# Kernel tuning notes

Hardware: AMD Instinct MI355X
Metric: run time of the kernel (lower is better)

Reference implementation:

```python
import jax, jax.numpy as jnp
import numpy as np

USER_NUM = 100000
ITEM_NUM = 50000
N = USER_NUM + ITEM_NUM
D = 64
NNZ = 2400000
B = 4096
NLEVEL = 3
LEAF = 32
HID = 256
NCLS = 2
NLAYERS = 2
EPS = 0.1
TAU = 0.2


def _l2norm(x, axis=-1):
    return x / jnp.clip(jnp.linalg.norm(x, axis=axis, keepdims=True), 1e-12)


def setup_inputs():
    key = jax.random.key(0)
    ks = jax.random.split(key, 32)
    def w(k, shape):
        fan = shape[-2] if len(shape) >= 2 else shape[-1]
        return jax.random.normal(k, shape, jnp.float32) / np.sqrt(fan)
    z = lambda *s: jnp.zeros(s, jnp.float32)
    return {
        "ego_emb": w(ks[0], (N, D)),
        "gc_w": w(ks[1], (NLAYERS, D, D)), "gc_b": z(NLAYERS, D),
        "bi_w": w(ks[2], (NLAYERS, D, D)), "bi_b": z(NLAYERS, D),
        "uh_w": w(ks[3], (NLEVEL, D, D)), "uh_b": z(NLEVEL, D),
        "ih_w": w(ks[4], (NLEVEL, D, D)), "ih_b": z(NLEVEL, D),
        "ud_w1": w(ks[5], (NLEVEL, D, HID)), "ud_b1": z(NLEVEL, HID),
        "ud_w2": w(ks[6], (NLEVEL, HID, LEAF)), "ud_b2": z(NLEVEL, LEAF),
        "id_w1": w(ks[7], (NLEVEL, D, HID)), "id_b1": z(NLEVEL, HID),
        "id_w2": w(ks[8], (NLEVEL, HID, LEAF)), "id_b2": z(NLEVEL, LEAF),
        "q_w": w(ks[9], (LEAF, LEAF)), "q_b": z(LEAF),
        "k_w": w(ks[10], (LEAF, LEAF)), "k_b": z(LEAF),
        "v_w": w(ks[11], (LEAF, LEAF)), "v_b": z(LEAF),
        "dg_w1": w(ks[12], (NLEVEL * LEAF, D)), "dg_b1": z(D),
        "dg_w2": w(ks[13], (D, D)), "dg_b2": z(D),
        "pr_w": w(ks[14], (D, NCLS)), "pr_b": z(NCLS),
        "adj_vals": jax.random.uniform(ks[15], (NNZ,), jnp.float32) / 16.0,
        "hier_skills": jax.random.uniform(ks[16], (B, NLEVEL * LEAF), jnp.float32),
        "user_id": jax.random.randint(ks[17], (B,), 0, USER_NUM),
        "item_id": jax.random.randint(ks[18], (B,), 0, ITEM_NUM),
        "adj_rows": jax.random.randint(ks[19], (NNZ,), 0, N),
        "adj_cols": jax.random.randint(ks[20], (NNZ,), 0, N),
    }


def _sam(x, q_w, q_b, k_w, k_b, v_w, v_b):
    # x: [B, S, d], single-head self-attention (n_heads=1)
    d = x.shape[-1]
    q = x @ q_w + q_b
    k = x @ k_w + k_b
    v = x @ v_w + v_b
    scores = jnp.einsum('bsd,btd->bst', q, k) / jnp.sqrt(jnp.float32(d))
    attn = jax.nn.softmax(scores, axis=-1)  # softmax over key axis t
    return jnp.einsum('bst,btd->bsd', attn, v)


def _cl_loss(v1, v2):
    n1 = _l2norm(v1)
    n2 = _l2norm(v2)
    pos = jnp.exp(jnp.sum(n1 * n2, -1) / TAU)
    ttl = jnp.sum(jnp.exp(n1 @ n2.T / TAU), axis=1)
    return jnp.mean(-jnp.log(pos / ttl))


def _cl_module(recs, key):
    # recs: [L, B, LEAF]
    noise = jax.random.uniform(key, recs.shape, recs.dtype)
    recs_new = recs + jnp.sign(recs) * _l2norm(noise) * EPS
    return jnp.mean(jax.vmap(_cl_loss)(recs, recs_new))


def reference(ego_emb, gc_w, gc_b, bi_w, bi_b, uh_w, uh_b, ih_w, ih_b,
              ud_w1, ud_b1, ud_w2, ud_b2, id_w1, id_b1, id_w2, id_b2,
              q_w, q_b, k_w, k_b, v_w, v_b, dg_w1, dg_b1, dg_w2, dg_b2,
              pr_w, pr_b, adj_vals, hier_skills, user_id, item_id,
              adj_rows, adj_cols):
    # ---- NGCF propagation: sparse adj matmul + bi-interaction ----
    E = ego_emb
    E_sum = ego_emb
    for l in range(NLAYERS):
        side = jax.ops.segment_sum(adj_vals[:, None] * E[adj_cols], adj_rows,
                                   num_segments=N)  # spmm(adj_norm, E)
        sum_e = jax.nn.leaky_relu(side @ gc_w[l] + gc_b[l])
        bi_e = jax.nn.leaky_relu((E * side) @ bi_w[l] + bi_b[l])
        E = _l2norm(sum_e + bi_e)  # dropout -> identity (eval)
        E_sum = E_sum + E
    ue = E_sum[:USER_NUM][user_id]   # [B, D]
    ie = E_sum[USER_NUM:][item_id]   # [B, D]
    # ---- hierarchy projections + disentangled encoders (stacked over levels) ----
    u_reps = jnp.tanh(jnp.einsum('bd,lde->lbe', ue, uh_w) + uh_b[:, None, :])
    i_reps = jnp.tanh(jnp.einsum('bd,lde->lbe', ie, ih_w) + ih_b[:, None, :])
    u_recs = jnp.einsum('lbh,lhk->lbk',
                        jnp.tanh(jnp.einsum('lbd,ldh->lbh', u_reps, ud_w1) + ud_b1[:, None, :]),
                        ud_w2) + ud_b2[:, None, :]  # [L, B, LEAF]
    i_recs = jnp.einsum('lbh,lhk->lbk',
                        jnp.tanh(jnp.einsum('lbd,ldh->lbh', i_reps, id_w1) + id_b1[:, None, :]),
                        id_w2) + id_b2[:, None, :]
    # ---- self-attention across levels ----
    u_att = _sam(u_recs.transpose(1, 0, 2), q_w, q_b, k_w, k_b, v_w, v_b)  # [B, L, LEAF]
    i_att = _sam(i_recs.transpose(1, 0, 2), q_w, q_b, k_w, k_b, v_w, v_b)
    # ---- contrastive losses (detached in original via torch.Tensor(...)) ----
    kc = jax.random.split(jax.random.key(42), 2)
    cl = _cl_module(u_att.transpose(1, 0, 2), kc[0]) + _cl_module(i_att.transpose(1, 0, 2), kc[1])
    cl = jax.lax.stop_gradient(cl)
    # ---- diagnosis head ----
    skills = hier_skills.reshape(B, NLEVEL, LEAF)
    diag = ((jax.nn.sigmoid(u_att) - jax.nn.sigmoid(i_att)) * skills).reshape(B, NLEVEL * LEAF)
    h = jnp.tanh(diag @ dg_w1 + dg_b1) @ dg_w2 + dg_b2  # dropout -> identity (eval)
    out = jax.nn.softmax(h @ pr_w + pr_b, axis=-1)
    return (out, cl)
```

## Files before the change

kernel.cpp:

```cpp
#include <hip/hip_runtime.h>
#include <stdint.h>
#include <math.h>

#define USER_N 100000
#define NODE_N 150000
#define DD 64
#define NNZE 2400000
#define BB 4096
#define NLV 3
#define LF 32
#define HALF_SZ 196608u
#define NTILE 586
#define NSUB 8
#define SCAP 1024
#define EPB 4096
#define LCAP 5120

typedef __attribute__((ext_vector_type(8))) short bf16x8;
typedef __attribute__((ext_vector_type(4))) float f32x4;
typedef __attribute__((ext_vector_type(2))) float f32x2;

#define XCC_ID_IMM 63508

__host__ __device__ inline void tf_block(uint32_t k0, uint32_t k1, uint32_t& x0, uint32_t& x1) {
  uint32_t ks[3] = {k0, k1, k0 ^ k1 ^ 0x1BD11BDAu};
  x0 += ks[0]; x1 += ks[1];
  const int R0[4] = {13, 15, 26, 6};
  const int R1[4] = {17, 29, 16, 24};
#pragma unroll
  for (int i = 0; i < 5; ++i) {
    const int* R = (i & 1) ? R1 : R0;
#pragma unroll
    for (int j = 0; j < 4; ++j) {
      x0 += x1;
      x1 = (x1 << R[j]) | (x1 >> (32 - R[j]));
      x1 ^= x0;
    }
    x0 += ks[(i + 1) % 3];
    x1 += ks[(i + 2) % 3] + (uint32_t)(i + 1);
  }
}

__device__ inline float tf_uniform(uint32_t ka, uint32_t kb, uint32_t m) {
  uint32_t x0, x1;
  bool first = m < HALF_SZ;
  if (first) { x0 = m; x1 = m + HALF_SZ; } else { x0 = m - HALF_SZ; x1 = m; }
  tf_block(ka, kb, x0, x1);
  uint32_t bits = first ? x0 : x1;
  return __uint_as_float((bits >> 9) | 0x3f800000u) - 1.0f;
}

__device__ inline unsigned short f2bf(float x) {
  uint32_t b = __float_as_uint(x);
  return (unsigned short)((b + 0x7FFFu + ((b >> 16) & 1u)) >> 16);
}

__device__ inline unsigned char f2fp8(float x) {
  return (unsigned char)(__builtin_amdgcn_cvt_pk_fp8_f32(x, x, 0, false) & 0xFF);
}

__device__ inline void fp8_fma(float4& acc, uint2 rec, uint32_t wrd) {
  float vv = __uint_as_float(rec.y);
  f32x2 lo = __builtin_amdgcn_cvt_pk_f32_fp8((int)wrd, false);
  f32x2 hi = __builtin_amdgcn_cvt_pk_f32_fp8((int)wrd, true);
  acc.x = fmaf(vv, lo.x, acc.x);
  acc.y = fmaf(vv, lo.y, acc.y);
  acc.z = fmaf(vv, hi.x, acc.z);
  acc.w = fmaf(vv, hi.y, acc.w);
}

__global__ __launch_bounds__(256) void k_init(
    const float* __restrict__ ego, uint32_t* __restrict__ E8,
    const float* __restrict__ uh_w, const float* __restrict__ ud_w1,
    const float* __restrict__ ud_w2, const float* __restrict__ ih_w,
    const float* __restrict__ id_w1, const float* __restrict__ id_w2,
    unsigned short* __restrict__ s1t, unsigned short* __restrict__ s2t,
    unsigned short* __restrict__ s3t, int* __restrict__ cursor,
    float* __restrict__ clbuf) {
  if (blockIdx.x >= 10047) {
    int i = (blockIdx.x - 10047) * 256 + threadIdx.x;
    if (i < NTILE * NSUB * 16) cursor[i] = 0;
    if (i == 0) { clbuf[0] = 0.f; ((int*)clbuf)[1] = 0; }
    return;
  }
  if (blockIdx.x < 9375) {
    int i = blockIdx.x * 256 + threadIdx.x;
    float4 v = ((const float4*)ego)[i];
    int w01 = __builtin_amdgcn_cvt_pk_fp8_f32(v.x, v.y, 0, false);
    int w = __builtin_amdgcn_cvt_pk_fp8_f32(v.z, v.w, w01, true);
    E8[i] = (uint32_t)w;
    return;
  }
  int i = (blockIdx.x - 9375) * 256 + threadIdx.x;
  if (i < 24576) {
    int sl = i >> 12, r = i & 4095, e = r >> 6, d = r & 63;
    const float* src = (sl >= 3 ? ih_w : uh_w);
    int l = sl % 3;
    s1t[i] = f2bf(src[l * 4096 + d * 64 + e]);
  } else if (i < 24576 + 98304) {
    int j = i - 24576;
    int sl = j >> 14, r = j & 16383, e = r >> 6, d = r & 63;
    const float* src = (sl >= 3 ? id_w1 : ud_w1);
    int l = sl % 3;
    s2t[j] = f2bf(src[l * 16384 + d * 256 + e]);
  } else if (i < 172032) {
    int j = i - 24576 - 98304;
    int sl = j >> 13, r = j & 8191, e = r >> 8, d = r & 255;
    const float* src = (sl >= 3 ? id_w2 : ud_w2);
    int l = sl % 3;
    s3t[j] = f2bf(src[l * 8192 + d * 32 + e]);
  }
}

__global__ __launch_bounds__(256) void k_scatter_t(const int* __restrict__ rows,
                                                   const int* __restrict__ cols,
                                                   const float* __restrict__ vals,
                                                   int* __restrict__ cursor,
                                                   uint2* __restrict__ sedge_r) {
  __shared__ int cnt[NTILE];
  __shared__ int binbase[NTILE];
  __shared__ int gbase[NTILE];
  __shared__ int partial[256];
  __shared__ uint2 staged[EPB];
  __shared__ unsigned short tileof[EPB];
  int t = threadIdx.x;
  for (int i = t; i < NTILE; i += 256) cnt[i] = 0;
  __syncthreads();
  int ebase = blockIdx.x * EPB;
  int r[16], rk[16];
#pragma unroll
  for (int j = 0; j < 16; ++j) {
    int e = ebase + j * 256 + t;
    r[j] = (e < NNZE) ? rows[e] : -1;
    rk[j] = (r[j] >= 0) ? atomicAdd(&cnt[r[j] >> 8], 1) : 0;
  }
  __syncthreads();
  int b0 = t * 3;
  int own = (b0 < NTILE) ? ((NTILE - b0 < 3) ? (NTILE - b0) : 3) : 0;
  int s0 = 0;
  for (int k = 0; k < own; ++k) s0 += cnt[b0 + k];
  partial[t] = s0;
  __syncthreads();
  for (int off = 1; off < 256; off <<= 1) {
    int add = (t >= off) ? partial[t - off] : 0;
    __syncthreads();
    partial[t] += add;
    __syncthreads();
  }
  int excl = partial[t] - s0;
  unsigned myx = __builtin_amdgcn_s_getreg(XCC_ID_IMM) & (NSUB - 1);
  {
    int run = excl;
    for (int k = 0; k < own; ++k) {
      int b = b0 + k;
      int c = cnt[b];
      binbase[b] = run;
      gbase[b] = c ? atomicAdd(&cursor[(b * NSUB + (int)myx) * 16], c) : 0;
      run += c;
    }
  }
  __syncthreads();
#pragma unroll
  for (int j = 0; j < 16; ++j) {
    if (r[j] < 0) continue;
    int e = ebase + j * 256 + t;
    int tile = r[j] >> 8;
    int pos = binbase[tile] + rk[j];
    staged[pos] = make_uint2((uint32_t)cols[e] | ((uint32_t)(r[j] & 255) << 18),
                             __float_as_uint(vals[e]));
    tileof[pos] = (unsigned short)tile;
  }
  __syncthreads();
  int nrec = NNZE - ebase;
  if (nrec > EPB) nrec = EPB;
  for (int i = t; i < nrec; i += 256) {
    int tile = tileof[i];
    int q = i - binbase[tile];
    int p = gbase[tile] + q;
    uint2 rec = staged[i];
    if (p < SCAP) {
      sedge_r[(size_t)(tile * NSUB + (int)myx) * SCAP + p] = rec;
    } else {
#pragma unroll 1
      for (int att = 1; att < NSUB; ++att) {
        int seg = tile * NSUB + (int)((myx + att) & (NSUB - 1));
        int p2 = atomicAdd(&cursor[seg * 16], 1);
        if (p2 < SCAP) { sedge_r[(size_t)seg * SCAP + p2] = rec; break; }
      }
    }
  }
}

__global__ __launch_bounds__(256) void k_sort_t(const uint2* __restrict__ sedge_r,
                                                const int* __restrict__ cursor,
                                                uint2* __restrict__ sedge,
                                                int* __restrict__ row_start) {
  __shared__ int hist[256], buf[256], curs[256];
  __shared__ int obase_s;
  __shared__ uint2 staged[LCAP];
  int t = threadIdx.x;
  int tile = blockIdx.x;
  if (t == 0) obase_s = 0;
  hist[t] = 0;
  __syncthreads();
  int ob = 0;
  for (int i = t; i < tile * NSUB; i += 256) {
    int c = cursor[i * 16];
    ob += (c < SCAP) ? c : SCAP;
  }
  if (ob) atomicAdd(&obase_s, ob);
  int segcnt[NSUB];
#pragma unroll
  for (int x = 0; x < NSUB; ++x) {
    int c = cursor[(tile * NSUB + x) * 16];
    segcnt[x] = (c < SCAP) ? c : SCAP;
  }
#pragma unroll 1
  for (int x = 0; x < NSUB; ++x) {
    const uint2* sp = sedge_r + (size_t)(tile * NSUB + x) * SCAP;
    for (int i = t; i < segcnt[x]; i += 256)
      atomicAdd(&hist[sp[i].x >> 18], 1);
  }
  __syncthreads();
  int obase = obase_s;
  int v = hist[t];
  buf[t] = v;
  __syncthreads();
  for (int off = 1; off < 256; off <<= 1) {
    int add = (t >= off) ? buf[t - off] : 0;
    __syncthreads();
    buf[t] += add;
    __syncthreads();
  }
  int total = buf[255];
  int excl = buf[t] - v;
  curs[t] = excl;
  int row = tile * 256 + t;
  if (row < NODE_N) row_start[row] = obase + excl;
  if (tile == NTILE - 1 && t == 0) row_start[NODE_N] = NNZE;
  __syncthreads();
#pragma unroll 1
  for (int x = 0; x < NSUB; ++x) {
    const uint2* sp = sedge_r + (size_t)(tile * NSUB + x) * SCAP;
    for (int i = t; i < segcnt[x]; i += 256) {
      uint2 rec = sp[i];
      int rl = rec.x >> 18;
      int p = atomicAdd(&curs[rl], 1);
      uint2 outrec = make_uint2(rec.x & 0x3FFFFu, rec.y);
      if (p < LCAP) staged[p] = outrec;
      else sedge[obase + p] = outrec;
    }
  }
  __syncthreads();
  int n = (total < LCAP) ? total : LCAP;
  for (int i = t; i < n; i += 256)
    sedge[obase + i] = staged[i];
}

__global__ __launch_bounds__(256) void k_spmm(const uint32_t* __restrict__ E8,
                                              const uint2* __restrict__ sedge,
                                              const int* __restrict__ row_start,
                                              unsigned short* __restrict__ side16,
                                              unsigned short* __restrict__ p16) {
  int r = blockIdx.x * 4 + (threadIdx.x >> 6);
  int lane = threadIdx.x & 63;
  int g = lane >> 4;
  int q = lane & 15;
  int rs = row_start[r], re = row_start[r + 1];
  float4 acc = make_float4(0.f, 0.f, 0.f, 0.f);
  int e = rs;
  for (; e + 16 <= re; e += 16) {
    uint2 e0 = sedge[e + g];
    uint2 e1 = sedge[e + 4 + g];
    uint2 e2 = sedge[e + 8 + g];
    uint2 e3 = sedge[e + 12 + g];
    uint32_t a0 = E8[(size_t)e0.x * 16 + q];
    uint32_t a1 = E8[(size_t)e1.x * 16 + q];
    uint32_t a2 = E8[(size_t)e2.x * 16 + q];
    uint32_t a3 = E8[(size_t)e3.x * 16 + q];
    fp8_fma(acc, e0, a0);
    fp8_fma(acc, e1, a1);
    fp8_fma(acc, e2, a2);
    fp8_fma(acc, e3, a3);
  }
  for (; e + 8 <= re; e += 8) {
    uint2 e0 = sedge[e + g];
    uint2 e1 = sedge[e + 4 + g];
    uint32_t a0 = E8[(size_t)e0.x * 16 + q];
    uint32_t a1 = E8[(size_t)e1.x * 16 + q];
    fp8_fma(acc, e0, a0);
    fp8_fma(acc, e1, a1);
  }
  for (; e + 4 <= re; e += 4) {
    uint2 e0 = sedge[e + g];
    uint32_t a0 = E8[(size_t)e0.x * 16 + q];
    fp8_fma(acc, e0, a0);
  }
  for (; e < re; ++e) {
    if (g == (e & 3)) {
      uint2 e0 = sedge[e];
      uint32_t a0 = E8[(size_t)e0.x * 16 + q];
      fp8_fma(acc, e0, a0);
    }
  }
#pragma unroll
  for (int off = 16; off <= 32; off <<= 1) {
    acc.x += __shfl_xor(acc.x, off, 64);
    acc.y += __shfl_xor(acc.y, off, 64);
    acc.z += __shfl_xor(acc.z, off, 64);
    acc.w += __shfl_xor(acc.w, off, 64);
  }
  if (g == 0) {
    uint32_t ew = E8[(size_t)r * 16 + q];
    f32x2 elo = __builtin_amdgcn_cvt_pk_f32_fp8((int)ew, false);
    f32x2 ehi = __builtin_amdgcn_cvt_pk_f32_fp8((int)ew, true);
    ushort4 s16, pp;
    s16.x = f2bf(acc.x); s16.y = f2bf(acc.y); s16.z = f2bf(acc.z); s16.w = f2bf(acc.w);
    pp.x = f2bf(acc.x * elo.x); pp.y = f2bf(acc.y * elo.y);
    pp.z = f2bf(acc.z * ehi.x); pp.w = f2bf(acc.w * ehi.y);
    *(ushort4*)&side16[(size_t)r * DD + q * 4] = s16;
    *(ushort4*)&p16[(size_t)r * DD + q * 4] = pp;
  }
}

__global__ __launch_bounds__(256) void k_transform(const float* __restrict__ gw,
                                                   const float* __restrict__ gb,
                                                   const float* __restrict__ bw,
                                                   const float* __restrict__ bb,
                                                   const unsigned short* __restrict__ side16,
                                                   const unsigned short* __restrict__ p16,
                                                   float* __restrict__ Eout,
                                                   unsigned char* __restrict__ E8b) {
  int t = threadIdx.x;
  int wv = t >> 6, lane = t & 63;
  int n = lane & 15, quad = lane >> 4;
  bf16x8 wg[4][2], wb[4][2];
  float gbl[4], bbl[4];
#pragma unroll
  for (int c = 0; c < 4; ++c) {
    gbl[c] = gb[c * 16 + n];
    bbl[c] = bb[c * 16 + n];
#pragma unroll
    for (int h = 0; h < 2; ++h) {
#pragma unroll
      for (int j = 0; j < 8; ++j) {
        int k = h * 32 + quad * 8 + j;
        wg[c][h][j] = (short)f2bf(gw[k * 64 + c * 16 + n]);
        wb[c][h][j] = (short)f2bf(bw[k * 64 + c * 16 + n]);
      }
    }
  }
  const f32x4 z = {0.f, 0.f, 0.f, 0.f};
  for (int tile = blockIdx.x * 4 + wv; tile < NODE_N / 16; tile += gridDim.x * 4) {
    int i0 = tile * 16;
    bf16x8 as0 = *(const bf16x8*)&side16[(size_t)(i0 + n) * DD + quad * 8];
    bf16x8 as1 = *(const bf16x8*)&side16[(size_t)(i0 + n) * DD + 32 + quad * 8];
    bf16x8 ap0 = *(const bf16x8*)&p16[(size_t)(i0 + n) * DD + quad * 8];
    bf16x8 ap1 = *(const bf16x8*)&p16[(size_t)(i0 + n) * DD + 32 + quad * 8];
    float v[4][4];
    float sq0 = 0.f, sq1 = 0.f, sq2 = 0.f, sq3 = 0.f;
#pragma unroll
    for (int c = 0; c < 4; ++c) {
      f32x4 ag = __builtin_amdgcn_mfma_f32_16x16x32_bf16(as0, wg[c][0], z, 0, 0, 0);
      ag = __builtin_amdgcn_mfma_f32_16x16x32_bf16(as1, wg[c][1], ag, 0, 0, 0);
      f32x4 ab = __builtin_amdgcn_mfma_f32_16x16x32_bf16(ap0, wb[c][0], z, 0, 0, 0);
      ab = __builtin_amdgcn_mfma_f32_16x16x32_bf16(ap1, wb[c][1], ab, 0, 0, 0);
#pragma unroll
      for (int r = 0; r < 4; ++r) {
        float a1 = ag[r] + gbl[c];
        a1 = (a1 > 0.f) ? a1 : 0.01f * a1;
        float a2 = ab[r] + bbl[c];
        a2 = (a2 > 0.f) ? a2 : 0.01f * a2;
        float vv = a1 + a2;
        v[c][r] = vv;
        if (r == 0) sq0 += vv * vv;
        else if (r == 1) sq1 += vv * vv;
        else if (r == 2) sq2 += vv * vv;
        else sq3 += vv * vv;
      }
    }
#pragma unroll
    for (int off = 1; off < 16; off <<= 1) {
      sq0 += __shfl_xor(sq0, off, 64);
      sq1 += __shfl_xor(sq1, off, 64);
      sq2 += __shfl_xor(sq2, off, 64);
      sq3 += __shfl_xor(sq3, off, 64);
    }
    float inv0 = 1.f / fmaxf(sqrtf(sq0), 1e-12f);
    float inv1 = 1.f / fmaxf(sqrtf(sq1), 1e-12f);
    float inv2 = 1.f / fmaxf(sqrtf(sq2), 1e-12f);
    float inv3 = 1.f / fmaxf(sqrtf(sq3), 1e-12f);
#pragma unroll
    for (int c = 0; c < 4; ++c) {
      float vn0 = v[c][0] * inv0;
      float vn1 = v[c][1] * inv1;
      float vn2 = v[c][2] * inv2;
      float vn3 = v[c][3] * inv3;
      size_t o0 = (size_t)(i0 + quad * 4 + 0) * DD + c * 16 + n;
      size_t o1 = o0 + DD, o2 = o1 + DD, o3 = o2 + DD;
      Eout[o0] = vn0; Eout[o1] = vn1; Eout[o2] = vn2; Eout[o3] = vn3;
      E8b[o0] = f2fp8(vn0); E8b[o1] = f2fp8(vn1);
      E8b[o2] = f2fp8(vn2); E8b[o3] = f2fp8(vn3);
    }
  }
}

__global__ __launch_bounds__(256) void k_encoder6(
    const float* __restrict__ ego, const float* __restrict__ E1,
    const float* __restrict__ E2, const int* __restrict__ uid,
    const int* __restrict__ iid,
    const unsigned short* __restrict__ s1t, const unsigned short* __restrict__ s2t,
    const unsigned short* __restrict__ s3t,
    const float* __restrict__ uh_b, const float* __restrict__ ud_b1,
    const float* __restrict__ ud_b2, const float* __restrict__ ih_b,
    const float* __restrict__ id_b1, const float* __restrict__ id_b2,
    float* __restrict__ recs_u, float* __restrict__ recs_i) {
  __shared__ unsigned short X[32][72];
  __shared__ unsigned short R1[32][64];
  __shared__ unsigned short T[32][256];
  int t = threadIdx.x;
  int w = t >> 6, lane = t & 63;
  int n = lane & 15, quad = lane >> 4;
  int trow = w & 1;
  int cg = w >> 1;
  int r0 = blockIdx.x * 32;
  int l = blockIdx.y, side = blockIdx.z;
  int sl = side * 3 + l;
  const float* hb = side ? ih_b : uh_b;
  const float* bb1 = side ? id_b1 : ud_b1;
  const float* bb2 = side ? id_b2 : ud_b2;
  float* recs = side ? recs_i : recs_u;
  const f32x4 z = {0.f, 0.f, 0.f, 0.f};

  {
    int row = t >> 3;
    int c0 = (t & 7) * 8;
    int node = side ? (USER_N + iid[r0 + row]) : uid[r0 + row];
    const float* pe = ego + (size_t)node * 64 + c0;
    const float* p1 = E1 + (size_t)node * 64 + c0;
    const float* p2 = E2 + (size_t)node * 64 + c0;
#pragma unroll
    for (int j = 0; j < 8; ++j)
      X[row][c0 + j] = f2bf(pe[j] + p1[j] + p2[j]);
  }
  __syncthreads();

  {
    bf16x8 a0 = *(const bf16x8*)&X[trow * 16 + n][quad * 8];
    bf16x8 a1 = *(const bf16x8*)&X[trow * 16 + n][32 + quad * 8];
    const unsigned short* Wt = s1t + (size_t)sl * 4096;
#pragma unroll
    for (int cc = 0; cc < 2; ++cc) {
      int cb = cg * 2 + cc;
      bf16x8 wb0 = *(const bf16x8*)&Wt[(size_t)(cb * 16 + n) * 64 + quad * 8];
      bf16x8 wb1 = *(const bf16x8*)&Wt[(size_t)(cb * 16 + n) * 64 + 32 + quad * 8];
      f32x4 acc = __builtin_amdgcn_mfma_f32_16x16x32_bf16(a0, wb0, z, 0, 0, 0);
      acc = __builtin_amdgcn_mfma_f32_16x16x32_bf16(a1, wb1, acc, 0, 0, 0);
      float bias = hb[l * 64 + cb * 16 + n];
#pragma unroll
      for (int r = 0; r < 4; ++r)
        R1[trow * 16 + quad * 4 + r][cb * 16 + n] = f2bf(tanhf(acc[r] + bias));
    }
  }
  __syncthreads();

  {
    bf16x8 a0 = *(const bf16x8*)&R1[trow * 16 + n][quad * 8];
    bf16x8 a1 = *(const bf16x8*)&R1[trow * 16 + n][32 + quad * 8];
    const unsigned short* Wt = s2t + (size_t)sl * 16384;
#pragma unroll
    for (int cc = 0; cc < 8; ++cc) {
      int cb = cg * 8 + cc;
      bf16x8 wb0 = *(const bf16x8*)&Wt[(size_t)(cb * 16 + n) * 64 + quad * 8];
      bf16x8 wb1 = *(const bf16x8*)&Wt[(size_t)(cb * 16 + n) * 64 + 32 + quad * 8];
      f32x4 acc = __builtin_amdgcn_mfma_f32_16x16x32_bf16(a0, wb0, z, 0, 0, 0);
      acc = __builtin_amdgcn_mfma_f32_16x16x32_bf16(a1, wb1, acc, 0, 0, 0);
      float bias = bb1[l * 256 + cb * 16 + n];
#pragma unroll
      for (int r = 0; r < 4; ++r)
        T[trow * 16 + quad * 4 + r][cb * 16 + n] = f2bf(tanhf(acc[r] + bias));
    }
  }
  __syncthreads();

  {
    const unsigned short* Wt = s3t + (size_t)sl * 8192;
    f32x4 acc = z;
#pragma unroll
    for (int h = 0; h < 8; ++h) {
      bf16x8 a = *(const bf16x8*)&T[trow * 16 + n][h * 32 + quad * 8];
      bf16x8 b = *(const bf16x8*)&Wt[(size_t)(cg * 16 + n) * 256 + h * 32 + quad * 8];
      acc = __builtin_amdgcn_mfma_f32_16x16x32_bf16(a, b, acc, 0, 0, 0);
    }
    float bias = bb2[l * 32 + cg * 16 + n];
#pragma unroll
    for (int r = 0; r < 4; ++r)
      recs[((size_t)l * BB + (r0 + trow * 16 + quad * 4 + r)) * 32 + cg * 16 + n] =
          acc[r] + bias;
  }
}

__global__ __launch_bounds__(256) void k_attnz(const float* __restrict__ recs_u,
                                               const float* __restrict__ recs_i,
                                               const float* __restrict__ qw, const float* __restrict__ qb,
                                               const float* __restrict__ kw, const float* __restrict__ kb,
                                               const float* __restrict__ vw, const float* __restrict__ vb,
                                               uint32_t ku0, uint32_t ku1, uint32_t ki0, uint32_t ki1,
                                               float* __restrict__ att_u, float* __restrict__ att_i,
                                               unsigned short* __restrict__ n1b,
                                               unsigned short* __restrict__ n2b,
                                               float* __restrict__ posdot) {
  int side = blockIdx.y;
  const float* recs = side ? recs_i : recs_u;
  float* att = side ? att_i : att_u;
  uint32_t ka = side ? ki0 : ku0;
  uint32_t kb2 = side ? ki1 : ku1;
  int t = threadIdx.x;
  int b = blockIdx.x * 8 + (t >> 5);
  int d = t & 31;
  float x0 = recs[((size_t)0 * BB + b) * 32 + d];
  float x1 = recs[((size_t)1 * BB + b) * 32 + d];
  float x2 = recs[((size_t)2 * BB + b) * 32 + d];
  float q0 = qb[d], q1 = q0, q2 = q0;
  float c0 = kb[d], c1 = c0, c2 = c0;
  float v0 = vb[d], v1 = v0, v2 = v0;
#pragma unroll 4
  for (int kk = 0; kk < 32; ++kk) {
    float xa = __shfl(x0, kk, 32);
    float xb = __shfl(x1, kk, 32);
    float xc = __shfl(x2, kk, 32);
    float wq = qw[kk * 32 + d], wk = kw[kk * 32 + d], wv = vw[kk * 32 + d];
    q0 += xa * wq; q1 += xb * wq; q2 += xc * wq;
    c0 += xa * wk; c1 += xb * wk; c2 += xc * wk;
    v0 += xa * wv; v1 += xb * wv; v2 += xc * wv;
  }
  float qs[3] = {q0, q1, q2}, ks[3] = {c0, c1, c2}, vs[3] = {v0, v1, v2};
  float sc[3][3];
#pragma unroll
  for (int s = 0; s < 3; ++s)
#pragma unroll
    for (int u = 0; u < 3; ++u) {
      float p = qs[s] * ks[u];
#pragma unroll
      for (int off = 16; off; off >>= 1) p += __shfl_xor(p, off, 32);
      sc[s][u] = p * 0.17677669529663687f;
    }
#pragma unroll
  for (int s = 0; s < 3; ++s) {
    float m = fmaxf(sc[s][0], fmaxf(sc[s][1], sc[s][2]));
    float e0 = __expf(sc[s][0] - m), e1 = __expf(sc[s][1] - m), e2 = __expf(sc[s][2] - m);
    float inv = 1.f / (e0 + e1 + e2);
    float r = (e0 * vs[0] + e1 * vs[1] + e2 * vs[2]) * inv;
    att[(size_t)b * 96 + s * 32 + d] = r;
    float ss = r * r;
#pragma unroll
    for (int off = 16; off; off >>= 1) ss += __shfl_xor(ss, off, 32);
    float nv1 = r / fmaxf(sqrtf(ss), 1e-12f);
    uint32_t mm = ((uint32_t)(s * BB + b)) * 32u + (uint32_t)d;
    float u = tf_uniform(ka, kb2, mm);
    float us = u * u;
#pragma unroll
    for (int off = 16; off; off >>= 1) us += __shfl_xor(us, off, 32);
    float un = u / fmaxf(sqrtf(us), 1e-12f);
    float sgn = (r > 0.f) ? 1.f : ((r < 0.f) ? -1.f : 0.f);
    float rn = r + sgn * un * 0.1f;
    float s2 = rn * rn;
#pragma unroll
    for (int off = 16; off; off >>= 1) s2 += __shfl_xor(s2, off, 32);
    float nv2 = rn / fmaxf(sqrtf(s2), 1e-12f);
    float pd = nv1 * nv2;
#pragma unroll
    for (int off = 16; off; off >>= 1) pd += __shfl_xor(pd, off, 32);
    int g = side * (NLV * BB) + s * BB + b;
    size_t o = (size_t)g * 32 + d;
    n1b[o] = f2bf(nv1);
    n2b[o] = f2bf(nv2);
    if (d == 0) posdot[g] = pd;
  }
}

__global__ __launch_bounds__(256) void k_ttl(const unsigned short* __restrict__ n1b,
                                             const unsigned short* __restrict__ n2b,
                                             const float* __restrict__ posdot,
                                             float* __restrict__ clbuf,
                                             float* __restrict__ outp) {
  __shared__ float ws[4];
  int t = threadIdx.x;
  int wv = t >> 6, lane = t & 63;
  int sl = blockIdx.x >> 6;
  int istripe = blockIdx.x & 63;
  int i0 = istripe * 64 + wv * 16;
  const unsigned short* ab = n1b + (size_t)sl * BB * 32;
  const unsigned short* bb = n2b + (size_t)sl * BB * 32;
  int m = lane & 15, quad = lane >> 4;
  bf16x8 afrag = *(const bf16x8*)&ab[(size_t)(i0 + m) * 32 + quad * 8];
  float r0a = 0.f, r1a = 0.f, r2a = 0.f, r3a = 0.f;
  f32x4 z = {0.f, 0.f, 0.f, 0.f};
  for (int jt = 0; jt < 256; jt += 4) {
    bf16x8 b0 = *(const bf16x8*)&bb[((size_t)((jt + 0) * 16 + m)) * 32 + quad * 8];
    bf16x8 b1 = *(const bf16x8*)&bb[((size_t)((jt + 1) * 16 + m)) * 32 + quad * 8];
    bf16x8 b2 = *(const bf16x8*)&bb[((size_t)((jt + 2) * 16 + m)) * 32 + quad * 8];
    bf16x8 b3 = *(const bf16x8*)&bb[((size_t)((jt + 3) * 16 + m)) * 32 + quad * 8];
    f32x4 s0 = __builtin_amdgcn_mfma_f32_16x16x32_bf16(afrag, b0, z, 0, 0, 0);
    f32x4 s1 = __builtin_amdgcn_mfma_f32_16x16x32_bf16(afrag, b1, z, 0, 0, 0);
    f32x4 s2 = __builtin_amdgcn_mfma_f32_16x16x32_bf16(afrag, b2, z, 0, 0, 0);
    f32x4 s3 = __builtin_amdgcn_mfma_f32_16x16x32_bf16(afrag, b3, z, 0, 0, 0);
    r0a += __expf(s0.x * 5.f) + __expf(s1.x * 5.f) + __expf(s2.x * 5.f) + __expf(s3.x * 5.f);
    r1a += __expf(s0.y * 5.f) + __expf(s1.y * 5.f) + __expf(s2.y * 5.f) + __expf(s3.y * 5.f);
    r2a += __expf(s0.z * 5.f) + __expf(s1.z * 5.f) + __expf(s2.z * 5.f) + __expf(s3.z * 5.f);
    r3a += __expf(s0.w * 5.f) + __expf(s1.w * 5.f) + __expf(s2.w * 5.f) + __expf(s3.w * 5.f);
  }
#pragma unroll
  for (int off = 1; off < 16; off <<= 1) {
    r0a += __shfl_xor(r0a, off, 64);
    r1a += __shfl_xor(r1a, off, 64);
    r2a += __shfl_xor(r2a, off, 64);
    r3a += __shfl_xor(r3a, off, 64);
  }
  float part = 0.f;
  if (m == 0) {
    int rbase = sl * BB + i0 + quad * 4;
    part = (logf(r0a) - posdot[rbase + 0] * 5.0f)
         + (logf(r1a) - posdot[rbase + 1] * 5.0f)
         + (logf(r2a) - posdot[rbase + 2] * 5.0f)
         + (logf(r3a) - posdot[rbase + 3] * 5.0f);
  }
#pragma unroll
  for (int off = 1; off < 64; off <<= 1)
    part += __shfl_xor(part, off, 64);
  if (lane == 0) ws[wv] = part;
  __syncthreads();
  if (t == 0) {
    float blk = ws[0] + ws[1] + ws[2] + ws[3];
    atomicAdd(&clbuf[0], blk);
    __threadfence();
    int done = atomicAdd((int*)&clbuf[1], 1);
    if (done == 383) {
      float total = atomicAdd(&clbuf[0], 0.0f);
      outp[2 * BB] = total * (1.f / 12288.f);
    }
  }
}

__global__ __launch_bounds__(256) void k_head(const float* __restrict__ att_u,
                                              const float* __restrict__ att_i,
                                              const float* __restrict__ skills,
                                              const float* __restrict__ w1, const float* __restrict__ b1,
                                              const float* __restrict__ w2, const float* __restrict__ b2,
                                              const float* __restrict__ pw, const float* __restrict__ pb,
                                              float* __restrict__ outp) {
  __shared__ float diag[4][96], t1[4][64];
  int t = threadIdx.x;
  int w = t >> 6, lane = t & 63;
  int b = blockIdx.x * 4 + w;
  for (int j = lane; j < 96; j += 64) {
    float su = 1.f / (1.f + __expf(-att_u[(size_t)b * 96 + j]));
    float si = 1.f / (1.f + __expf(-att_i[(size_t)b * 96 + j]));
    diag[w][j] = (su - si) * skills[(size_t)b * 96 + j];
  }
  __syncthreads();
  float a = b1[lane];
#pragma unroll 8
  for (int j = 0; j < 96; ++j) a += diag[w][j] * w1[j * 64 + lane];
  t1[w][lane] = tanhf(a);
  __syncthreads();
  float h = b2[lane];
#pragma unroll 8
  for (int kk = 0; kk < 64; ++kk) h += t1[w][kk] * w2[kk * 64 + lane];
  float p0 = h * pw[lane * 2 + 0];
  float p1 = h * pw[lane * 2 + 1];
#pragma unroll
  for (int off = 32; off; off >>= 1) {
    p0 += __shfl_xor(p0, off, 64);
    p1 += __shfl_xor(p1, off, 64);
  }
  if (lane == 0) {
    float l0 = p0 + pb[0], l1 = p1 + pb[1];
    float m = fmaxf(l0, l1);
    float e0 = __expf(l0 - m), e1 = __expf(l1 - m);
    float inv = 1.f / (e0 + e1);
    outp[(size_t)b * 2 + 0] = e0 * inv;
    outp[(size_t)b * 2 + 1] = e1 * inv;
  }
}

extern "C" void kernel_launch(void* const* d_in, const int* in_sizes, int n_in,
                              void* d_out, int out_size, void* d_ws, size_t ws_size,
                              hipStream_t stream) {
  const float* ego    = (const float*)d_in[0];
  const float* gc_w   = (const float*)d_in[1];
  const float* gc_b   = (const float*)d_in[2];
  const float* bi_w   = (const float*)d_in[3];
  const float* bi_b   = (const float*)d_in[4];
  const float* uh_w   = (const float*)d_in[5];
  const float* uh_b   = (const float*)d_in[6];
  const float* ih_w   = (const float*)d_in[7];
  const float* ih_b   = (const float*)d_in[8];
  const float* ud_w1  = (const float*)d_in[9];
  const float* ud_b1  = (const float*)d_in[10];
  const float* ud_w2  = (const float*)d_in[11];
  const float* ud_b2  = (const float*)d_in[12];
  const float* id_w1  = (const float*)d_in[13];
  const float* id_b1  = (const float*)d_in[14];
  const float* id_w2  = (const float*)d_in[15];
  const float* id_b2  = (const float*)d_in[16];
  const float* q_w    = (const float*)d_in[17];
  const float* q_b    = (const float*)d_in[18];
  const float* k_w    = (const float*)d_in[19];
  const float* k_b    = (const float*)d_in[20];
  const float* v_w    = (const float*)d_in[21];
  const float* v_b    = (const float*)d_in[22];
  const float* dg_w1  = (const float*)d_in[23];
  const float* dg_b1  = (const float*)d_in[24];
  const float* dg_w2  = (const float*)d_in[25];
  const float* dg_b2  = (const float*)d_in[26];
  const float* pr_w   = (const float*)d_in[27];
  const float* pr_b   = (const float*)d_in[28];
  const float* adj_vals = (const float*)d_in[29];
  const float* skills = (const float*)d_in[30];
  const int* user_id  = (const int*)d_in[31];
  const int* item_id  = (const int*)d_in[32];
  const int* adj_rows = (const int*)d_in[33];
  const int* adj_cols = (const int*)d_in[34];
  float* outp = (float*)d_out;

  char* w = (char*)d_ws;
  auto alloc = [&](size_t bytes) -> char* {
    char* p = w;
    w += (bytes + 255) & ~(size_t)255;
    return p;
  };
  float* E1     = (float*)alloc((size_t)NODE_N * DD * 4);
  float* E2     = (float*)alloc((size_t)NODE_N * DD * 4);
  uint32_t* E8  = (uint32_t*)alloc((size_t)NODE_N * DD);
  unsigned short* side16 = (unsigned short*)alloc((size_t)NODE_N * DD * 2);
  unsigned short* p16    = (unsigned short*)alloc((size_t)NODE_N * DD * 2);
  uint2* sedge_r= (uint2*)alloc((size_t)NTILE * NSUB * SCAP * 8);
  uint2* sedge  = (uint2*)alloc((size_t)NNZE * 8);
  int*   cursor = (int*)  alloc((size_t)NTILE * NSUB * 16 * 4);
  int*   row_start = (int*)alloc((size_t)(NODE_N + 1) * 4);
  float* posdot = (float*)alloc((size_t)6 * BB * 4);
  float* clbuf  = (float*)alloc(256);
  unsigned short* s1t = (unsigned short*)alloc((size_t)24576 * 2);
  unsigned short* s2t = (unsigned short*)alloc((size_t)98304 * 2);
  unsigned short* s3t = (unsigned short*)alloc((size_t)49152 * 2);

  char* ap = (char*)sedge_r;
  auto alias = [&](size_t bytes) -> char* {
    char* p = ap;
    ap += (bytes + 255) & ~(size_t)255;
    return p;
  };
  float* recs_u = (float*)alias((size_t)NLV * BB * 32 * 4);
  float* recs_i = (float*)alias((size_t)NLV * BB * 32 * 4);
  float* att_u  = (float*)alias((size_t)BB * 96 * 4);
  float* att_i  = (float*)alias((size_t)BB * 96 * 4);
  unsigned short* n1b = (unsigned short*)alias((size_t)6 * BB * 32 * 2);
  unsigned short* n2b = (unsigned short*)alias((size_t)6 * BB * 32 * 2);

  uint32_t a0 = 0, a1 = 2, b0 = 1, b1 = 3;
  tf_block(0u, 42u, a0, a1);
  tf_block(0u, 42u, b0, b1);
  uint32_t ku0 = a0, ku1 = b0;
  uint32_t ki0 = a1, ki1 = b1;

  k_init<<<10341, 256, 0, stream>>>(ego, E8, uh_w, ud_w1, ud_w2,
                                    ih_w, id_w1, id_w2, s1t, s2t, s3t,
                                    cursor, clbuf);
  k_scatter_t<<<(NNZE + EPB - 1) / EPB, 256, 0, stream>>>(adj_rows, adj_cols, adj_vals,
                                                          cursor, sedge_r);
  k_sort_t<<<NTILE, 256, 0, stream>>>(sedge_r, cursor, sedge, row_start);

  float* Ebufs[2] = {E1, E2};
  for (int l = 0; l < 2; ++l) {
    k_spmm<<<37500, 256, 0, stream>>>(E8, sedge, row_start, side16, p16);
    k_transform<<<1172, 256, 0, stream>>>(gc_w + l * 4096, gc_b + l * 64,
                                          bi_w + l * 4096, bi_b + l * 64,
                                          side16, p16, Ebufs[l], (unsigned char*)E8);
  }

  dim3 ge(128, 3, 2);
  k_encoder6<<<ge, 256, 0, stream>>>(ego, E1, E2, user_id, item_id,
                                     s1t, s2t, s3t,
                                     uh_b, ud_b1, ud_b2, ih_b, id_b1, id_b2,
                                     recs_u, recs_i);

  dim3 ga(512, 2);
  k_attnz<<<ga, 256, 0, stream>>>(recs_u, recs_i, q_w, q_b, k_w, k_b, v_w, v_b,
                                  ku0, ku1, ki0, ki1,
                                  att_u, att_i, n1b, n2b, posdot);

  k_ttl<<<384, 256, 0, stream>>>(n1b, n2b, posdot, clbuf, outp);

  k_head<<<1024, 256, 0, stream>>>(att_u, att_i, skills, dg_w1, dg_b1, dg_w2, dg_b2,
                                   pr_w, pr_b, outp);
}
```

Before: 515.1 us.

## Fuse SpMM aggregation with dense layer transform via shared-memory staging

Merges the sparse aggregation kernel and the MFMA transform kernel into one kernel per layer. Each block aggregates 16 rows into LDS as bf16 and then runs the 64x64 transform and L2 normalization directly on them. This removes the side16/p16 round trip through global memory. Weights are pre-transposed to bf16 once in the init kernel, and the fp8 embedding buffer is double-buffered so the fused kernel never reads rows it is also writing. In exchange, each wave handles four rows serially and the block must synchronize before the MFMA phase, which can reduce latency hiding in the gather.

```diff
diff --git a/kernel.cpp b/kernel.cpp
--- a/kernel.cpp
+++ b/kernel.cpp
@@ -74,11 +74,12 @@
     const float* __restrict__ uh_w, const float* __restrict__ ud_w1,
     const float* __restrict__ ud_w2, const float* __restrict__ ih_w,
     const float* __restrict__ id_w1, const float* __restrict__ id_w2,
+    const float* __restrict__ gc_w, const float* __restrict__ bi_w,
     unsigned short* __restrict__ s1t, unsigned short* __restrict__ s2t,
-    unsigned short* __restrict__ s3t, int* __restrict__ cursor,
-    float* __restrict__ clbuf) {
-  if (blockIdx.x >= 10047) {
-    int i = (blockIdx.x - 10047) * 256 + threadIdx.x;
+    unsigned short* __restrict__ s3t, unsigned short* __restrict__ twt,
+    int* __restrict__ cursor, float* __restrict__ clbuf) {
+  if (blockIdx.x >= 10111) {
+    int i = (blockIdx.x - 10111) * 256 + threadIdx.x;
     if (i < NTILE * NSUB * 16) cursor[i] = 0;
     if (i == 0) { clbuf[0] = 0.f; ((int*)clbuf)[1] = 0; }
     return;
@@ -109,6 +110,17 @@
     const float* src = (sl >= 3 ? id_w2 : ud_w2);
     int l = sl % 3;
     s3t[j] = f2bf(src[l * 8192 + d * 32 + e]);
+  } else if (i < 172032 + 16384) {
+    int j = i - 172032;
+    int m = j >> 13;
+    int rest = j & 8191;
+    int l = rest >> 12;
+    int e = rest & 4095;
+    int jj = e & 7, quad = (e >> 3) & 3, h = (e >> 5) & 1;
+    int n = (e >> 6) & 15, c = e >> 10;
+    int k = h * 32 + quad * 8 + jj;
+    const float* src = m ? bi_w : gc_w;
+    twt[j] = f2bf(src[l * 4096 + k * 64 + c * 16 + n]);
   }
 }
 
@@ -257,151 +269,137 @@
     sedge[obase + i] = staged[i];
 }
 
-__global__ __launch_bounds__(256) void k_spmm(const uint32_t* __restrict__ E8,
-                                              const uint2* __restrict__ sedge,
-                                              const int* __restrict__ row_start,
-                                              unsigned short* __restrict__ side16,
-                                              unsigned short* __restrict__ p16) {
-  int r = blockIdx.x * 4 + (threadIdx.x >> 6);
-  int lane = threadIdx.x & 63;
-  int g = lane >> 4;
-  int q = lane & 15;
-  int rs = row_start[r], re = row_start[r + 1];
-  float4 acc = make_float4(0.f, 0.f, 0.f, 0.f);
-  int e = rs;
-  for (; e + 16 <= re; e += 16) {
-    uint2 e0 = sedge[e + g];
-    uint2 e1 = sedge[e + 4 + g];
-    uint2 e2 = sedge[e + 8 + g];
-    uint2 e3 = sedge[e + 12 + g];
-    uint32_t a0 = E8[(size_t)e0.x * 16 + q];
-    uint32_t a1 = E8[(size_t)e1.x * 16 + q];
-    uint32_t a2 = E8[(size_t)e2.x * 16 + q];
-    uint32_t a3 = E8[(size_t)e3.x * 16 + q];
-    fp8_fma(acc, e0, a0);
-    fp8_fma(acc, e1, a1);
-    fp8_fma(acc, e2, a2);
-    fp8_fma(acc, e3, a3);
-  }
-  for (; e + 8 <= re; e += 8) {
-    uint2 e0 = sedge[e + g];
-    uint2 e1 = sedge[e + 4 + g];
-    uint32_t a0 = E8[(size_t)e0.x * 16 + q];
-    uint32_t a1 = E8[(size_t)e1.x * 16 + q];
-    fp8_fma(acc, e0, a0);
-    fp8_fma(acc, e1, a1);
-  }
-  for (; e + 4 <= re; e += 4) {
-    uint2 e0 = sedge[e + g];
-    uint32_t a0 = E8[(size_t)e0.x * 16 + q];
-    fp8_fma(acc, e0, a0);
-  }
-  for (; e < re; ++e) {
-    if (g == (e & 3)) {
-      uint2 e0 = sedge[e];
-      uint32_t a0 = E8[(size_t)e0.x * 16 + q];
-      fp8_fma(acc, e0, a0);
-    }
-  }
-#pragma unroll
-  for (int off = 16; off <= 32; off <<= 1) {
-    acc.x += __shfl_xor(acc.x, off, 64);
-    acc.y += __shfl_xor(acc.y, off, 64);
-    acc.z += __shfl_xor(acc.z, off, 64);
-    acc.w += __shfl_xor(acc.w, off, 64);
-  }
-  if (g == 0) {
-    uint32_t ew = E8[(size_t)r * 16 + q];
-    f32x2 elo = __builtin_amdgcn_cvt_pk_f32_fp8((int)ew, false);
-    f32x2 ehi = __builtin_amdgcn_cvt_pk_f32_fp8((int)ew, true);
-    ushort4 s16, pp;
-    s16.x = f2bf(acc.x); s16.y = f2bf(acc.y); s16.z = f2bf(acc.z); s16.w = f2bf(acc.w);
-    pp.x = f2bf(acc.x * elo.x); pp.y = f2bf(acc.y * elo.y);
-    pp.z = f2bf(acc.z * ehi.x); pp.w = f2bf(acc.w * ehi.y);
-    *(ushort4*)&side16[(size_t)r * DD + q * 4] = s16;
-    *(ushort4*)&p16[(size_t)r * DD + q * 4] = pp;
-  }
-}
-
-__global__ __launch_bounds__(256) void k_transform(const float* __restrict__ gw,
-                                                   const float* __restrict__ gb,
-                                                   const float* __restrict__ bw,
-                                                   const float* __restrict__ bb,
-                                                   const unsigned short* __restrict__ side16,
-                                                   const unsigned short* __restrict__ p16,
-                                                   float* __restrict__ Eout,
-                                                   unsigned char* __restrict__ E8b) {
+__global__ __launch_bounds__(256) void k_spmmt(const uint32_t* __restrict__ E8in,
+                                               const uint2* __restrict__ sedge,
+                                               const int* __restrict__ row_start,
+                                               const unsigned short* __restrict__ gwt,
+                                               const float* __restrict__ gb,
+                                               const unsigned short* __restrict__ bwt,
+                                               const float* __restrict__ bb,
+                                               float* __restrict__ Eout,
+                                               unsigned char* __restrict__ E8out) {
+  __shared__ unsigned short sS[16][72];
+  __shared__ unsigned short sP[16][72];
+  __shared__ float sqp[4][16];
   int t = threadIdx.x;
   int wv = t >> 6, lane = t & 63;
+  int i0 = blockIdx.x * 16;
+  {
+    int g = lane >> 4;
+    int q = lane & 15;
+#pragma unroll 1
+    for (int rr = 0; rr < 4; ++rr) {
+      int r = i0 + wv * 4 + rr;
+      int rs = row_start[r], re = row_start[r + 1];
+      float4 acc = make_float4(0.f, 0.f, 0.f, 0.f);
+      int e = rs;
+      for (; e + 16 <= re; e += 16) {
+        uint2 e0 = sedge[e + g];
+        uint2 e1 = sedge[e + 4 + g];
+        uint2 e2 = sedge[e + 8 + g];
+        uint2 e3 = sedge[e + 12 + g];
+        uint32_t a0 = E8in[(size_t)e0.x * 16 + q];
+        uint32_t a1 = E8in[(size_t)e1.x * 16 + q];
+        uint32_t a2 = E8in[(size_t)e2.x * 16 + q];
+        uint32_t a3 = E8in[(size_t)e3.x * 16 + q];
+        fp8_fma(acc, e0, a0);
+        fp8_fma(acc, e1, a1);
+        fp8_fma(acc, e2, a2);
+        fp8_fma(acc, e3, a3);
+      }
+      for (; e + 8 <= re; e += 8) {
+        uint2 e0 = sedge[e + g];
+        uint2 e1 = sedge[e + 4 + g];
+        uint32_t a0 = E8in[(size_t)e0.x * 16 + q];
+        uint32_t a1 = E8in[(size_t)e1.x * 16 + q];
+        fp8_fma(acc, e0, a0);
+        fp8_fma(acc, e1, a1);
+      }
+      for (; e + 4 <= re; e += 4) {
+        uint2 e0 = sedge[e + g];
+        uint32_t a0 = E8in[(size_t)e0.x * 16 + q];
+        fp8_fma(acc, e0, a0);
+      }
+      for (; e < re; ++e) {
+        if (g == (e & 3)) {
+          uint2 e0 = sedge[e];
+          uint32_t a0 = E8in[(size_t)e0.x * 16 + q];
+          fp8_fma(acc, e0, a0);
+        }
+      }
+#pragma unroll
+      for (int off = 16; off <= 32; off <<= 1) {
+        acc.x += __shfl_xor(acc.x, off, 64);
+        acc.y += __shfl_xor(acc.y, off, 64);
+        acc.z += __shfl_xor(acc.z, off, 64);
+        acc.w += __shfl_xor(acc.w, off, 64);
+      }
+      if (g == 0) {
+        uint32_t ew = E8in[(size_t)r * 16 + q];
+        f32x2 elo = __builtin_amdgcn_cvt_pk_f32_fp8((int)ew, false);
+        f32x2 ehi = __builtin_amdgcn_cvt_pk_f32_fp8((int)ew, true);
+        int lr = wv * 4 + rr;
+        sS[lr][q * 4 + 0] = f2bf(acc.x);
+        sS[lr][q * 4 + 1] = f2bf(acc.y);
+        sS[lr][q * 4 + 2] = f2bf(acc.z);
+        sS[lr][q * 4 + 3] = f2bf(acc.w);
+        sP[lr][q * 4 + 0] = f2bf(acc.x * elo.x);
+        sP[lr][q * 4 + 1] = f2bf(acc.y * elo.y);
+        sP[lr][q * 4 + 2] = f2bf(acc.z * ehi.x);
+        sP[lr][q * 4 + 3] = f2bf(acc.w * ehi.y);
+      }
+    }
+  }
+  __syncthreads();
   int n = lane & 15, quad = lane >> 4;
-  bf16x8 wg[4][2], wb[4][2];
-  float gbl[4], bbl[4];
-#pragma unroll
-  for (int c = 0; c < 4; ++c) {
-    gbl[c] = gb[c * 16 + n];
-    bbl[c] = bb[c * 16 + n];
-#pragma unroll
-    for (int h = 0; h < 2; ++h) {
-#pragma unroll
-      for (int j = 0; j < 8; ++j) {
-        int k = h * 32 + quad * 8 + j;
-        wg[c][h][j] = (short)f2bf(gw[k * 64 + c * 16 + n]);
-        wb[c][h][j] = (short)f2bf(bw[k * 64 + c * 16 + n]);
-      }
-    }
-  }
   const f32x4 z = {0.f, 0.f, 0.f, 0.f};
-  for (int tile = blockIdx.x * 4 + wv; tile < NODE_N / 16; tile += gridDim.x * 4) {
-    int i0 = tile * 16;
-    bf16x8 as0 = *(const bf16x8*)&side16[(size_t)(i0 + n) * DD + quad * 8];
-    bf16x8 as1 = *(const bf16x8*)&side16[(size_t)(i0 + n) * DD + 32 + quad * 8];
-    bf16x8 ap0 = *(const bf16x8*)&p16[(size_t)(i0 + n) * DD + quad * 8];
-    bf16x8 ap1 = *(const bf16x8*)&p16[(size_t)(i0 + n) * DD + 32 + quad * 8];
-    float v[4][4];
-    float sq0 = 0.f, sq1 = 0.f, sq2 = 0.f, sq3 = 0.f;
-#pragma unroll
-    for (int c = 0; c < 4; ++c) {
-      f32x4 ag = __builtin_amdgcn_mfma_f32_16x16x32_bf16(as0, wg[c][0], z, 0, 0, 0);
-      ag = __builtin_amdgcn_mfma_f32_16x16x32_bf16(as1, wg[c][1], ag, 0, 0, 0);
-      f32x4 ab = __builtin_amdgcn_mfma_f32_16x16x32_bf16(ap0, wb[c][0], z, 0, 0, 0);
-      ab = __builtin_amdgcn_mfma_f32_16x16x32_bf16(ap1, wb[c][1], ab, 0, 0, 0);
-#pragma unroll
-      for (int r = 0; r < 4; ++r) {
-        float a1 = ag[r] + gbl[c];
-        a1 = (a1 > 0.f) ? a1 : 0.01f * a1;
-        float a2 = ab[r] + bbl[c];
-        a2 = (a2 > 0.f) ? a2 : 0.01f * a2;
-        float vv = a1 + a2;
-        v[c][r] = vv;
-        if (r == 0) sq0 += vv * vv;
-        else if (r == 1) sq1 += vv * vv;
-        else if (r == 2) sq2 += vv * vv;
-        else sq3 += vv * vv;
-      }
-    }
-#pragma unroll
-    for (int off = 1; off < 16; off <<= 1) {
-      sq0 += __shfl_xor(sq0, off, 64);
-      sq1 += __shfl_xor(sq1, off, 64);
-      sq2 += __shfl_xor(sq2, off, 64);
-      sq3 += __shfl_xor(sq3, off, 64);
-    }
-    float inv0 = 1.f / fmaxf(sqrtf(sq0), 1e-12f);
-    float inv1 = 1.f / fmaxf(sqrtf(sq1), 1e-12f);
-    float inv2 = 1.f / fmaxf(sqrtf(sq2), 1e-12f);
-    float inv3 = 1.f / fmaxf(sqrtf(sq3), 1e-12f);
-#pragma unroll
-    for (int c = 0; c < 4; ++c) {
-      float vn0 = v[c][0] * inv0;
-      float vn1 = v[c][1] * inv1;
-      float vn2 = v[c][2] * inv2;
-      float vn3 = v[c][3] * inv3;
-      size_t o0 = (size_t)(i0 + quad * 4 + 0) * DD + c * 16 + n;
-      size_t o1 = o0 + DD, o2 = o1 + DD, o3 = o2 + DD;
-      Eout[o0] = vn0; Eout[o1] = vn1; Eout[o2] = vn2; Eout[o3] = vn3;
-      E8b[o0] = f2fp8(vn0); E8b[o1] = f2fp8(vn1);
-      E8b[o2] = f2fp8(vn2); E8b[o3] = f2fp8(vn3);
-    }
+  bf16x8 wg0 = *(const bf16x8*)&gwt[((size_t)(wv * 16 + n) * 2 + 0) * 32 + quad * 8];
+  bf16x8 wg1 = *(const bf16x8*)&gwt[((size_t)(wv * 16 + n) * 2 + 1) * 32 + quad * 8];
+  bf16x8 wb0 = *(const bf16x8*)&bwt[((size_t)(wv * 16 + n) * 2 + 0) * 32 + quad * 8];
+  bf16x8 wb1 = *(const bf16x8*)&bwt[((size_t)(wv * 16 + n) * 2 + 1) * 32 + quad * 8];
+  float gbl = gb[wv * 16 + n];
+  float bbl = bb[wv * 16 + n];
+  bf16x8 as0 = *(const bf16x8*)&sS[n][quad * 8];
+  bf16x8 as1 = *(const bf16x8*)&sS[n][32 + quad * 8];
+  bf16x8 ap0 = *(const bf16x8*)&sP[n][quad * 8];
+  bf16x8 ap1 = *(const bf16x8*)&sP[n][32 + quad * 8];
+  f32x4 ag = __builtin_amdgcn_mfma_f32_16x16x32_bf16(as0, wg0, z, 0, 0, 0);
+  ag = __builtin_amdgcn_mfma_f32_16x16x32_bf16(as1, wg1, ag, 0, 0, 0);
+  f32x4 ab = __builtin_amdgcn_mfma_f32_16x16x32_bf16(ap0, wb0, z, 0, 0, 0);
+  ab = __builtin_amdgcn_mfma_f32_16x16x32_bf16(ap1, wb1, ab, 0, 0, 0);
+  float v[4];
+  float sq[4];
+#pragma unroll
+  for (int r = 0; r < 4; ++r) {
+    float a1 = ag[r] + gbl;
+    a1 = (a1 > 0.f) ? a1 : 0.01f * a1;
+    float a2 = ab[r] + bbl;
+    a2 = (a2 > 0.f) ? a2 : 0.01f * a2;
+    float vv = a1 + a2;
+    v[r] = vv;
+    sq[r] = vv * vv;
+  }
+#pragma unroll
+  for (int off = 1; off < 16; off <<= 1) {
+    sq[0] += __shfl_xor(sq[0], off, 64);
+    sq[1] += __shfl_xor(sq[1], off, 64);
+    sq[2] += __shfl_xor(sq[2], off, 64);
+    sq[3] += __shfl_xor(sq[3], off, 64);
+  }
+  if (n == 0) {
+#pragma unroll
+    for (int r = 0; r < 4; ++r) sqp[wv][quad * 4 + r] = sq[r];
+  }
+  __syncthreads();
+#pragma unroll
+  for (int r = 0; r < 4; ++r) {
+    int row = quad * 4 + r;
+    float tot = sqp[0][row] + sqp[1][row] + sqp[2][row] + sqp[3][row];
+    float inv = 1.f / fmaxf(sqrtf(tot), 1e-12f);
+    float vn = v[r] * inv;
+    size_t o = (size_t)(i0 + row) * DD + wv * 16 + n;
+    Eout[o] = vn;
+    E8out[o] = f2fp8(vn);
   }
 }
 
@@ -732,9 +730,8 @@
   };
   float* E1     = (float*)alloc((size_t)NODE_N * DD * 4);
   float* E2     = (float*)alloc((size_t)NODE_N * DD * 4);
-  uint32_t* E8  = (uint32_t*)alloc((size_t)NODE_N * DD);
-  unsigned short* side16 = (unsigned short*)alloc((size_t)NODE_N * DD * 2);
-  unsigned short* p16    = (unsigned short*)alloc((size_t)NODE_N * DD * 2);
+  uint32_t* E8a = (uint32_t*)alloc((size_t)NODE_N * DD);
+  uint32_t* E8b = (uint32_t*)alloc((size_t)NODE_N * DD);
   uint2* sedge_r= (uint2*)alloc((size_t)NTILE * NSUB * SCAP * 8);
   uint2* sedge  = (uint2*)alloc((size_t)NNZE * 8);
   int*   cursor = (int*)  alloc((size_t)NTILE * NSUB * 16 * 4);
@@ -744,6 +741,7 @@
   unsigned short* s1t = (unsigned short*)alloc((size_t)24576 * 2);
   unsigned short* s2t = (unsigned short*)alloc((size_t)98304 * 2);
   unsigned short* s3t = (unsigned short*)alloc((size_t)49152 * 2);
+  unsigned short* twt = (unsigned short*)alloc((size_t)16384 * 2);
 
   char* ap = (char*)sedge_r;
   auto alias = [&](size_t bytes) -> char* {
@@ -764,20 +762,19 @@
   uint32_t ku0 = a0, ku1 = b0;
   uint32_t ki0 = a1, ki1 = b1;
 
-  k_init<<<10341, 256, 0, stream>>>(ego, E8, uh_w, ud_w1, ud_w2,
-                                    ih_w, id_w1, id_w2, s1t, s2t, s3t,
-                                    cursor, clbuf);
+  k_init<<<10405, 256, 0, stream>>>(ego, E8a, uh_w, ud_w1, ud_w2,
+                                    ih_w, id_w1, id_w2, gc_w, bi_w,
+                                    s1t, s2t, s3t, twt, cursor, clbuf);
   k_scatter_t<<<(NNZE + EPB - 1) / EPB, 256, 0, stream>>>(adj_rows, adj_cols, adj_vals,
                                                           cursor, sedge_r);
   k_sort_t<<<NTILE, 256, 0, stream>>>(sedge_r, cursor, sedge, row_start);
 
-  float* Ebufs[2] = {E1, E2};
-  for (int l = 0; l < 2; ++l) {
-    k_spmm<<<37500, 256, 0, stream>>>(E8, sedge, row_start, side16, p16);
-    k_transform<<<1172, 256, 0, stream>>>(gc_w + l * 4096, gc_b + l * 64,
-                                          bi_w + l * 4096, bi_b + l * 64,
-                                          side16, p16, Ebufs[l], (unsigned char*)E8);
-  }
+  k_spmmt<<<9375, 256, 0, stream>>>(E8a, sedge, row_start,
+                                    twt, gc_b, twt + 8192, bi_b,
+                                    E1, (unsigned char*)E8b);
+  k_spmmt<<<9375, 256, 0, stream>>>(E8b, sedge, row_start,
+                                    twt + 4096, gc_b + 64, twt + 12288, bi_b + 64,
+                                    E2, (unsigned char*)E8a);
 
   dim3 ge(128, 3, 2);
   k_encoder6<<<ge, 256, 0, stream>>>(ego, E1, E2, user_id, item_id,
```

Measured after the change: 499.9 us. 1.03x faster.
